# Optimization experiments

Measured on AMD Instinct MI355X. Metric: run time of the kernel, lower is better.

The kernel has to match this reference:

```python
import jax, jax.numpy as jnp
import numpy as np

B, N, F_IN, T = 16, 512, 32, 24
K, C_OUT = 3, 64


def setup_inputs() -> dict:
    key = jax.random.key(0)
    k1, k2, k3, k4 = jax.random.split(key, 4)
    X = jax.random.normal(k1, (B, N, F_IN, T), dtype=jnp.float32)
    s_a = jax.random.uniform(k2, (B, N, N), dtype=jnp.float32)
    cheb = jax.random.normal(k3, (K, N, N), dtype=jnp.float32)
    # Theta per nn.Parameter(K, c_in, c_out), kaiming-style scale
    Theta = jax.random.normal(k4, (K, F_IN, C_OUT), dtype=jnp.float32) * np.float32(np.sqrt(2.0 / F_IN))
    return {"X": X, "s_a": s_a, "cheb": cheb, "Theta": Theta}


def reference(X, s_a, cheb, Theta):
    # A[k,b,n,m] = T_k[n,m] * s_a[b,n,m]  (attention-masked Chebyshev polynomial)
    A = cheb[:, None, :, :] * s_a[None, :, :, :]  # [K,B,N,N]
    # torch: rhs = bmm(A.permute(0,2,1), X_t); out_t = sum_k rhs @ Theta_k
    # -> out[t,b,m,o] = sum_{k,n,f} A[k,b,n,m] * X[b,n,f,t] * Theta[k,f,o]
    out = jnp.einsum('kbnm,bnft,kfo->tbmo', A, X, Theta)  # [T,B,N,c_out]
    return jax.nn.relu(out)  # graph_conv_act_func == 'relu'
```

## Files before the change

### kernel.cpp

```cpp
#include <hip/hip_runtime.h>
#include <hip/hip_bf16.h>

#define B_ 16
#define N_ 512
#define F_ 32
#define T_ 24
#define K_ 3
#define C_ 64
#define FT_ 768
#define KF_ 96

typedef __attribute__((ext_vector_type(8))) short bf16x8;
typedef __attribute__((ext_vector_type(4))) float f32x4;

static __device__ __forceinline__ ushort f2b(float x) {
  uint u = __float_as_uint(x);
  return (ushort)((u + 0x7fffu + ((u >> 16) & 1u)) >> 16);
}
static __device__ __forceinline__ uint pk2(float a, float b) {
  return (uint)f2b(a) | ((uint)f2b(b) << 16);
}

#define GLOAD_LDS16(g, l)                                                     \
  __builtin_amdgcn_global_load_lds(                                           \
      (const __attribute__((address_space(1))) void*)(g),                     \
      (__attribute__((address_space(3))) void*)(l), 16, 0, 0)


__global__ __launch_bounds__(256) void prepX(const float* __restrict__ X,
                                             ushort* __restrict__ Xt2) {
  __shared__ ushort L[32 * FT_];
  const int b = blockIdx.y;
  const int n0 = blockIdx.x * 32;
  const int tid = threadIdx.x;

  const float* Xp = X + ((size_t)b * N_ + n0) * FT_;
#pragma unroll
  for (int it = 0; it < 24; ++it) {
    int idx = tid + it * 256;
    int row = idx / 192, c4 = idx % 192;
    float4 v = *(const float4*)(Xp + (size_t)row * FT_ + c4 * 4);
    uint2 p; p.x = pk2(v.x, v.y); p.y = pk2(v.z, v.w);
    *(uint2*)&L[row * FT_ + c4 * 4] = p;
  }
  __syncthreads();
#pragma unroll
  for (int j = 0; j < 3; ++j) {
    int ft2 = j * 256 + tid;
    int t = ft2 >> 5, f = ft2 & 31;
    int incol = f * T_ + t;
    ushort tmp[32];
#pragma unroll
    for (int r = 0; r < 32; ++r) tmp[r] = L[r * FT_ + incol];
    uint wv[16];
#pragma unroll
    for (int q = 0; q < 16; ++q)
      wv[q] = (uint)tmp[2 * q] | ((uint)tmp[2 * q + 1] << 16);
    ushort* op = Xt2 + ((size_t)b * FT_ + ft2) * N_ + n0;
#pragma unroll
    for (int q = 0; q < 4; ++q) {
      uint4 w; w.x = wv[4*q]; w.y = wv[4*q+1]; w.z = wv[4*q+2]; w.w = wv[4*q+3];
      *((uint4*)op + q) = w;
    }
  }
}

__global__ __launch_bounds__(256) void prepA(const float* __restrict__ SA,
                                             const float* __restrict__ CH,
                                             ushort* __restrict__ At) {
  const int kb = blockIdx.y;
  const int k = kb >> 4, b = kb & 15;
  const int m0 = (blockIdx.x & 7) * 64, n0 = (blockIdx.x >> 3) * 64;
  const int tid = threadIdx.x;
  const int ml = (tid & 15) * 4, nl = (tid >> 4) * 4;

  const float* cp = CH + ((size_t)k * N_ + n0 + nl) * N_ + m0 + ml;
  const float* sp = SA + ((size_t)b * N_ + n0 + nl) * N_ + m0 + ml;
  float4 p[4];
#pragma unroll
  for (int q = 0; q < 4; ++q) {
    float4 c = *(const float4*)(cp + (size_t)q * N_);
    float4 s = *(const float4*)(sp + (size_t)q * N_);
    p[q] = make_float4(c.x * s.x, c.y * s.y, c.z * s.z, c.w * s.w);
  }
  ushort* ob = At + (size_t)kb * N_ * N_ + (size_t)(m0 + ml) * N_ + n0 + nl;
#pragma unroll
  for (int s = 0; s < 4; ++s) {
    uint2 w;
    w.x = pk2(((const float*)&p[0])[s], ((const float*)&p[1])[s]);
    w.y = pk2(((const float*)&p[2])[s], ((const float*)&p[3])[s]);
    *(uint2*)(ob + (size_t)s * N_) = w;
  }
}

__global__ __launch_bounds__(256) void prepTh(const float* __restrict__ TH,
                                              ushort* __restrict__ Th2) {
  const int tid = threadIdx.x;
  const int o = tid & 63, g = tid >> 6;
#pragma unroll
  for (int q = 0; q < 24; ++q) {
    int kf = g * 24 + q;
    Th2[o * KF_ + kf] = f2b(TH[(size_t)kf * C_ + o]);
  }
}

__global__ __launch_bounds__(256, 2) void stage1(const ushort* __restrict__ Xt2,
                                                 const ushort* __restrict__ At,
                                                 ushort* __restrict__ R2) {
  __shared__ __align__(16) ushort Abuf[128 * 64];
  __shared__ __align__(16) ushort Bbuf[128 * 64];
  const int kb = blockIdx.y;
  const int k = kb >> 4, b = kb & 15;
  const int ft0 = (blockIdx.x >> 2) * 128;
  const int m0 = (blockIdx.x & 3) * 128;
  const int tid = threadIdx.x, lane = tid & 63, wid = tid >> 6;
  const int wft = (wid >> 1) * 64, wm = (wid & 1) * 64;

  const char* Xbase = (const char*)(Xt2 + ((size_t)b * FT_ + ft0) * N_);
  const char* Bbase = (const char*)(At + ((size_t)kb * N_ + m0) * N_);
  const int srow = lane >> 3;
  const int scol = (lane & 7) * 16;

  f32x4 acc[4][4];
#pragma unroll
  for (int i = 0; i < 4; ++i)
#pragma unroll
    for (int j = 0; j < 4; ++j) acc[i][j] = (f32x4){0.f, 0.f, 0.f, 0.f};

  for (int nb = 0; nb < 8; ++nb) {
    __syncthreads();
#pragma unroll
    for (int c = 0; c < 4; ++c) {
      const int s = wid * 4 + c;
      const size_t go = (size_t)(s * 8 + srow) * 1024 + nb * 128 + scol;
      GLOAD_LDS16(Xbase + go, (char*)Abuf + s * 1024);
      GLOAD_LDS16(Bbase + go, (char*)Bbuf + s * 1024);
    }
    __syncthreads();
#pragma unroll
    for (int kk = 0; kk < 2; ++kk) {
      const int cb = kk * 64 + (lane >> 4) * 16;
      bf16x8 af[4], bfv[4];
#pragma unroll
      for (int i = 0; i < 4; ++i)
        af[i] = *(const bf16x8*)((const char*)Abuf + (wft + i * 16 + (lane & 15)) * 128 + cb);
#pragma unroll
      for (int j = 0; j < 4; ++j)
        bfv[j] = *(const bf16x8*)((const char*)Bbuf + (wm + j * 16 + (lane & 15)) * 128 + cb);
#pragma unroll
      for (int i = 0; i < 4; ++i)
#pragma unroll
        for (int j = 0; j < 4; ++j)
          acc[i][j] = __builtin_amdgcn_mfma_f32_16x16x32_bf16(af[i], bfv[j], acc[i][j], 0, 0, 0);
    }
  }

  const int col = lane & 15, rg4 = (lane >> 4) * 4;
#pragma unroll
  for (int i = 0; i < 4; ++i) {
    const int rowl = wft + i * 16 + rg4;
    const int ft2 = ft0 + rowl;
    const int t = ft2 >> 5, f = ft2 & 31;
#pragma unroll
    for (int j = 0; j < 4; ++j) {
      const int m = m0 + wm + j * 16 + col;
      uint2 w;
      w.x = pk2(acc[i][j][0], acc[i][j][1]);
      w.y = pk2(acc[i][j][2], acc[i][j][3]);
      *(uint2*)(R2 + ((size_t)(b * T_ + t) * N_ + m) * KF_ + k * 32 + f) = w;
    }
  }
}

__global__ __launch_bounds__(256, 2) void stage2(const ushort* __restrict__ R2,
                                                 const ushort* __restrict__ Th2,
                                                 float* __restrict__ Out) {
  const int mh = blockIdx.x;
  const int t = blockIdx.y, b = blockIdx.z;
  const int tid = threadIdx.x, lane = tid & 63, wid = tid >> 6;
  const int m0w = mh * 256 + wid * 64;
  const int col = lane & 15, kc = (lane >> 4) * 8, rg4 = (lane >> 4) * 4;

  bf16x8 bfr[3][4];
#pragma unroll
  for (int ks = 0; ks < 3; ++ks)
#pragma unroll
    for (int j = 0; j < 4; ++j)
      bfr[ks][j] = *(const bf16x8*)(Th2 + (size_t)(j * 16 + col) * KF_ + ks * 32 + kc);

  const ushort* Rb = R2 + ((size_t)b * T_ + t) * N_ * KF_;
  float* Ob = Out + ((size_t)t * B_ + b) * N_ * C_;

#pragma unroll
  for (int i = 0; i < 4; ++i) {
    const int m = m0w + i * 16;
    bf16x8 af[3];
#pragma unroll
    for (int ks = 0; ks < 3; ++ks)
      af[ks] = *(const bf16x8*)(Rb + (size_t)(m + col) * KF_ + ks * 32 + kc);
    f32x4 acc[4];
#pragma unroll
    for (int j = 0; j < 4; ++j) acc[j] = (f32x4){0.f, 0.f, 0.f, 0.f};
#pragma unroll
    for (int ks = 0; ks < 3; ++ks)
#pragma unroll
      for (int j = 0; j < 4; ++j)
        acc[j] = __builtin_amdgcn_mfma_f32_16x16x32_bf16(af[ks], bfr[ks][j], acc[j], 0, 0, 0);
#pragma unroll
    for (int j = 0; j < 4; ++j)
#pragma unroll
      for (int r = 0; r < 4; ++r)
        Ob[(size_t)(m + rg4 + r) * C_ + j * 16 + col] = fmaxf(acc[j][r], 0.f);
  }
}

extern "C" void kernel_launch(void* const* d_in, const int* in_sizes, int n_in,
                              void* d_out, int out_size, void* d_ws, size_t ws_size,
                              hipStream_t stream) {
  const float* X  = (const float*)d_in[0];
  const float* SA = (const float*)d_in[1];
  const float* CH = (const float*)d_in[2];
  const float* TH = (const float*)d_in[3];
  float* Out = (float*)d_out;

  char* ws = (char*)d_ws;
  ushort* R2  = (ushort*)(ws);
  ushort* Xt2 = (ushort*)(ws + 37748736);
  ushort* At  = (ushort*)(ws + 37748736 + 12582912);
  ushort* Th2 = (ushort*)(ws + 37748736 + 12582912 + 25165824);

  prepX<<<dim3(16, 16), 256, 0, stream>>>(X, Xt2);
  prepA<<<dim3(64, 48), 256, 0, stream>>>(SA, CH, At);
  prepTh<<<1, 256, 0, stream>>>(TH, Th2);
  stage1<<<dim3(24, 48), 256, 0, stream>>>(Xt2, At, R2);
  stage2<<<dim3(2, 24, 16), 256, 0, stream>>>(R2, Th2, Out);
}
```

Baseline: 161.3 us.

## Double-buffer stage1 LDS with swizzle, split prepX grid, fuse Theta conversion into stage2

Stage1 now keeps two LDS buffers and issues the next tile's global-to-LDS loads before computing on the current one, so load latency overlaps MFMA work. Both the LDS store and read addresses are XOR-swizzled to cut bank conflicts. prepX runs three times as many blocks, each covering 8 timesteps, and uses a padded LDS tile. The separate prepTh kernel is removed and stage2 converts Theta to bf16 inline, which saves a launch but makes every block do strided fp32 loads of Theta. Double buffering doubles stage1 LDS use, which may lower occupancy.

```diff
diff --git a/kernel.cpp b/kernel.cpp
--- a/kernel.cpp
+++ b/kernel.cpp
@@ -27,41 +27,39 @@
       (__attribute__((address_space(3))) void*)(l), 16, 0, 0)
 
 
+#define XP_PAD 260
 __global__ __launch_bounds__(256) void prepX(const float* __restrict__ X,
                                              ushort* __restrict__ Xt2) {
-  __shared__ ushort L[32 * FT_];
+  __shared__ ushort L[32 * XP_PAD];
   const int b = blockIdx.y;
-  const int n0 = blockIdx.x * 32;
+  const int n0 = (blockIdx.x & 15) * 32;
+  const int fg = blockIdx.x >> 4;
   const int tid = threadIdx.x;
 
-  const float* Xp = X + ((size_t)b * N_ + n0) * FT_;
-#pragma unroll
-  for (int it = 0; it < 24; ++it) {
-    int idx = tid + it * 256;
-    int row = idx / 192, c4 = idx % 192;
-    float4 v = *(const float4*)(Xp + (size_t)row * FT_ + c4 * 4);
+  const float* Xp = X + ((size_t)b * N_ + n0) * FT_ + fg * 8;
+#pragma unroll
+  for (int it = 0; it < 8; ++it) {
+    int c = tid + it * 256;
+    int row = c >> 6, rem = c & 63;
+    int f = rem >> 1, half = rem & 1;
+    float4 v = *(const float4*)(Xp + (size_t)row * FT_ + f * 24 + half * 4);
     uint2 p; p.x = pk2(v.x, v.y); p.y = pk2(v.z, v.w);
-    *(uint2*)&L[row * FT_ + c4 * 4] = p;
+    *(uint2*)&L[row * XP_PAD + f * 8 + half * 4] = p;
   }
   __syncthreads();
-#pragma unroll
-  for (int j = 0; j < 3; ++j) {
-    int ft2 = j * 256 + tid;
-    int t = ft2 >> 5, f = ft2 & 31;
-    int incol = f * T_ + t;
-    ushort tmp[32];
-#pragma unroll
-    for (int r = 0; r < 32; ++r) tmp[r] = L[r * FT_ + incol];
-    uint wv[16];
-#pragma unroll
-    for (int q = 0; q < 16; ++q)
-      wv[q] = (uint)tmp[2 * q] | ((uint)tmp[2 * q + 1] << 16);
-    ushort* op = Xt2 + ((size_t)b * FT_ + ft2) * N_ + n0;
-#pragma unroll
-    for (int q = 0; q < 4; ++q) {
-      uint4 w; w.x = wv[4*q]; w.y = wv[4*q+1]; w.z = wv[4*q+2]; w.w = wv[4*q+3];
-      *((uint4*)op + q) = w;
-    }
+  const int ft2 = fg * 256 + tid;
+  const int f = tid & 31, dt = tid >> 5;
+  ushort a[32];
+#pragma unroll
+  for (int r = 0; r < 32; ++r) a[r] = L[r * XP_PAD + f * 8 + dt];
+  uint w[16];
+#pragma unroll
+  for (int q = 0; q < 16; ++q) w[q] = (uint)a[2 * q] | ((uint)a[2 * q + 1] << 16);
+  ushort* op = Xt2 + ((size_t)b * FT_ + ft2) * N_ + n0;
+#pragma unroll
+  for (int q = 0; q < 4; ++q) {
+    uint4 v; v.x = w[4*q]; v.y = w[4*q+1]; v.z = w[4*q+2]; v.w = w[4*q+3];
+    *((uint4*)op + q) = v;
   }
 }
 
@@ -93,22 +91,11 @@
   }
 }
 
-__global__ __launch_bounds__(256) void prepTh(const float* __restrict__ TH,
-                                              ushort* __restrict__ Th2) {
-  const int tid = threadIdx.x;
-  const int o = tid & 63, g = tid >> 6;
-#pragma unroll
-  for (int q = 0; q < 24; ++q) {
-    int kf = g * 24 + q;
-    Th2[o * KF_ + kf] = f2b(TH[(size_t)kf * C_ + o]);
-  }
-}
-
 __global__ __launch_bounds__(256, 2) void stage1(const ushort* __restrict__ Xt2,
                                                  const ushort* __restrict__ At,
                                                  ushort* __restrict__ R2) {
-  __shared__ __align__(16) ushort Abuf[128 * 64];
-  __shared__ __align__(16) ushort Bbuf[128 * 64];
+  __shared__ __align__(16) ushort Abuf[2][128 * 64];
+  __shared__ __align__(16) ushort Bbuf[2][128 * 64];
   const int kb = blockIdx.y;
   const int k = kb >> 4, b = kb & 15;
   const int ft0 = (blockIdx.x >> 2) * 128;
@@ -119,7 +106,7 @@
   const char* Xbase = (const char*)(Xt2 + ((size_t)b * FT_ + ft0) * N_);
   const char* Bbase = (const char*)(At + ((size_t)kb * N_ + m0) * N_);
   const int srow = lane >> 3;
-  const int scol = (lane & 7) * 16;
+  const int scolS = ((lane & 7) * 16) ^ (srow << 4);
 
   f32x4 acc[4][4];
 #pragma unroll
@@ -127,39 +114,49 @@
 #pragma unroll
     for (int j = 0; j < 4; ++j) acc[i][j] = (f32x4){0.f, 0.f, 0.f, 0.f};
 
+#define STAGE1_LOAD(bufi, nb)                                                  \
+  {                                                                            \
+    _Pragma("unroll")                                                          \
+    for (int c = 0; c < 4; ++c) {                                              \
+      const int s = wid * 4 + c;                                               \
+      const size_t go = (size_t)(s * 8 + srow) * 1024 + (nb) * 128 + scolS;    \
+      GLOAD_LDS16(Xbase + go, (char*)Abuf[bufi] + s * 1024);                   \
+      GLOAD_LDS16(Bbase + go, (char*)Bbuf[bufi] + s * 1024);                   \
+    }                                                                          \
+  }
+
+  STAGE1_LOAD(0, 0);
+  __syncthreads();
+
+  int cur = 0;
   for (int nb = 0; nb < 8; ++nb) {
-    __syncthreads();
-#pragma unroll
-    for (int c = 0; c < 4; ++c) {
-      const int s = wid * 4 + c;
-      const size_t go = (size_t)(s * 8 + srow) * 1024 + nb * 128 + scol;
-      GLOAD_LDS16(Xbase + go, (char*)Abuf + s * 1024);
-      GLOAD_LDS16(Bbase + go, (char*)Bbuf + s * 1024);
-    }
-    __syncthreads();
+    if (nb < 7) STAGE1_LOAD(cur ^ 1, nb + 1);
+    const char* Ab = (const char*)Abuf[cur];
+    const char* Bb = (const char*)Bbuf[cur];
 #pragma unroll
     for (int kk = 0; kk < 2; ++kk) {
-      const int cb = kk * 64 + (lane >> 4) * 16;
+      const int cb = (kk * 64 + (lane >> 4) * 16) ^ ((lane & 7) << 4);
       bf16x8 af[4], bfv[4];
 #pragma unroll
       for (int i = 0; i < 4; ++i)
-        af[i] = *(const bf16x8*)((const char*)Abuf + (wft + i * 16 + (lane & 15)) * 128 + cb);
+        af[i] = *(const bf16x8*)(Ab + (wft + i * 16 + (lane & 15)) * 128 + cb);
 #pragma unroll
       for (int j = 0; j < 4; ++j)
-        bfv[j] = *(const bf16x8*)((const char*)Bbuf + (wm + j * 16 + (lane & 15)) * 128 + cb);
+        bfv[j] = *(const bf16x8*)(Bb + (wm + j * 16 + (lane & 15)) * 128 + cb);
 #pragma unroll
       for (int i = 0; i < 4; ++i)
 #pragma unroll
         for (int j = 0; j < 4; ++j)
           acc[i][j] = __builtin_amdgcn_mfma_f32_16x16x32_bf16(af[i], bfv[j], acc[i][j], 0, 0, 0);
     }
+    __syncthreads();
+    cur ^= 1;
   }
 
   const int col = lane & 15, rg4 = (lane >> 4) * 4;
 #pragma unroll
   for (int i = 0; i < 4; ++i) {
-    const int rowl = wft + i * 16 + rg4;
-    const int ft2 = ft0 + rowl;
+    const int ft2 = ft0 + wft + i * 16 + rg4;
     const int t = ft2 >> 5, f = ft2 & 31;
 #pragma unroll
     for (int j = 0; j < 4; ++j) {
@@ -173,7 +170,7 @@
 }
 
 __global__ __launch_bounds__(256, 2) void stage2(const ushort* __restrict__ R2,
-                                                 const ushort* __restrict__ Th2,
+                                                 const float* __restrict__ TH,
                                                  float* __restrict__ Out) {
   const int mh = blockIdx.x;
   const int t = blockIdx.y, b = blockIdx.z;
@@ -185,8 +182,13 @@
 #pragma unroll
   for (int ks = 0; ks < 3; ++ks)
 #pragma unroll
-    for (int j = 0; j < 4; ++j)
-      bfr[ks][j] = *(const bf16x8*)(Th2 + (size_t)(j * 16 + col) * KF_ + ks * 32 + kc);
+    for (int j = 0; j < 4; ++j) {
+      const float* tp = TH + (size_t)(ks * 32 + kc) * C_ + j * 16 + col;
+      bf16x8 v;
+#pragma unroll
+      for (int q = 0; q < 8; ++q) v[q] = (short)f2b(tp[(size_t)q * C_]);
+      bfr[ks][j] = v;
+    }
 
   const ushort* Rb = R2 + ((size_t)b * T_ + t) * N_ * KF_;
   float* Ob = Out + ((size_t)t * B_ + b) * N_ * C_;
@@ -227,11 +229,9 @@
   ushort* R2  = (ushort*)(ws);
   ushort* Xt2 = (ushort*)(ws + 37748736);
   ushort* At  = (ushort*)(ws + 37748736 + 12582912);
-  ushort* Th2 = (ushort*)(ws + 37748736 + 12582912 + 25165824);
-
-  prepX<<<dim3(16, 16), 256, 0, stream>>>(X, Xt2);
+
+  prepX<<<dim3(48, 16), 256, 0, stream>>>(X, Xt2);
   prepA<<<dim3(64, 48), 256, 0, stream>>>(SA, CH, At);
-  prepTh<<<1, 256, 0, stream>>>(TH, Th2);
   stage1<<<dim3(24, 48), 256, 0, stream>>>(Xt2, At, R2);
-  stage2<<<dim3(2, 24, 16), 256, 0, stream>>>(R2, Th2, Out);
-}
+  stage2<<<dim3(2, 24, 16), 256, 0, stream>>>(R2, TH, Out);
+}
```

Measured after the change: 162.7 us. About the same (+0.9%).
